# Performance work log

Measured on AMD Instinct MI355X. Metric: run time of the kernel, lower is better.

The kernel has to match this reference:

```python
import jax, jax.numpy as jnp
import numpy as np

D_MODEL = 384
N_HEADS = 8
HEAD_DIM = D_MODEL // N_HEADS


def setup_inputs() -> dict:
    key = jax.random.key(0)
    ks = jax.random.split(key, 8)
    b, n = 2, 2048
    s = 0.02
    return {
        "x": jax.random.normal(ks[0], (b, n, D_MODEL), jnp.float32),
        "coords": jax.random.normal(ks[1], (b, n, 3), jnp.float32),
        "W_qkv": jax.random.normal(ks[2], (D_MODEL, 3 * D_MODEL), jnp.float32) * s,
        "b_qkv": jnp.zeros((3 * D_MODEL,), jnp.float32),
        "W_dist": jax.random.normal(ks[3], (1, N_HEADS), jnp.float32) * s,
        "b_dist": jnp.zeros((N_HEADS,), jnp.float32),
        "W_out": jax.random.normal(ks[4], (D_MODEL, D_MODEL), jnp.float32) * s,
        "b_out": jnp.zeros((D_MODEL,), jnp.float32),
    }


def reference(x, coords, W_qkv, b_qkv, W_dist, b_dist, W_out, b_out):
    b, n, _ = x.shape
    qkv = x @ W_qkv + b_qkv                       # (b, n, 3*d)
    q, k, v = jnp.split(qkv, 3, axis=-1)
    def heads(t):
        return t.reshape(b, n, N_HEADS, HEAD_DIM).transpose(0, 2, 1, 3)  # b h n d
    q, k, v = heads(q), heads(k), heads(v)
    attn = jnp.einsum('bhid,bhjd->bhij', q, k) / jnp.sqrt(jnp.float32(HEAD_DIM))
    # distance bias: ||c_i - c_j|| projected to heads (Linear(1, n_heads))
    diff = coords[:, :, None, :] - coords[:, None, :, :]   # (b, i, j, 3)
    dist = jnp.sqrt(jnp.sum(diff * diff, axis=-1))         # (b, i, j)
    dist_bias = dist[..., None] * W_dist[0] + b_dist       # (b, i, j, h)
    attn = attn + dist_bias.transpose(0, 3, 1, 2)          # (b, h, i, j)
    attn = jax.nn.softmax(attn, axis=-1)
    out = jnp.einsum('bhij,bhjd->bhid', attn, v)
    out = out.transpose(0, 2, 1, 3).reshape(b, n, D_MODEL)
    return out @ W_out + b_out
```

## Files before the change

kernel.cpp:

```cpp
#include <hip/hip_runtime.h>
#include <hip/hip_bf16.h>

#define NB 2
#define SEQ 2048
#define DM 384
#define NH 8
#define HD 48
#define QKVN 1152

typedef __hip_bfloat16 bf16;
typedef __attribute__((ext_vector_type(8))) short short8;
typedef __attribute__((ext_vector_type(4))) float float4v;
typedef __attribute__((ext_vector_type(16))) float f32x16;

static __device__ __forceinline__ float bf2f(bf16 v){ return __bfloat162float(v); }
static __device__ __forceinline__ float ldin(const void* p, size_t i, int isf){
    return isf ? ((const float*)p)[i] : bf2f(((const bf16*)p)[i]);
}
static __device__ __forceinline__ short f2b(float f){
    union { float f; unsigned u; } a; a.f = f;
    unsigned r = a.u + 0x7FFFu + ((a.u >> 16) & 1u);
    return (short)(r >> 16);
}
static __device__ __forceinline__ unsigned pk2(float a, float b){
    union { __hip_bfloat162 h; unsigned u; } r;
    r.h = __float22bfloat162_rn(float2{a, b});
    return r.u;
}
static __device__ __forceinline__ float bflo(unsigned u){
    union { unsigned u; float f; } a; a.u = u << 16; return a.f;
}
static __device__ __forceinline__ float bfhi(unsigned u){
    union { unsigned u; float f; } a; a.u = u & 0xFFFF0000u; return a.f;
}
static __device__ __forceinline__ short8 u4pack(unsigned w0, unsigned w1, unsigned w2, unsigned w3){
    union { unsigned u[4]; short8 s; } r; r.u[0]=w0; r.u[1]=w1; r.u[2]=w2; r.u[3]=w3; return r.s;
}
static __device__ __forceinline__ int detect_isf(const void* x){
    const unsigned short* xb = (const unsigned short*)x;
    int l = threadIdx.x & 63;
    union { unsigned u; float f; } a; a.u = ((unsigned)xb[2*l]) << 16;
    float ab = fabsf(a.f);
    int good = (a.f == 0.0f) || (ab > 9.765625e-4f && ab < 1024.0f);
    unsigned long long m = __ballot(good);
    return (__popcll(m) >= 32) ? 0 : 1;
}

__global__ __launch_bounds__(256) void k_prep(const void* __restrict__ x,
    const void* __restrict__ coords,
    const void* __restrict__ Wqkv, const void* __restrict__ Wout,
    const void* __restrict__ bqkv, const void* __restrict__ bout,
    const void* __restrict__ Wdist, const void* __restrict__ bdist,
    short* __restrict__ dist8, short* __restrict__ xb,
    short* __restrict__ WqT, short* __restrict__ WoT,
    float* __restrict__ bqf, float* __restrict__ bof,
    float* __restrict__ wdf, float* __restrict__ bdf)
{
    const int isf = detect_isf(x);
    const int t = threadIdx.x;
    const int b = blockIdx.x;
    if (b < 512) {
        const int bb = b >> 8;
        const int jg = (b >> 1) & 127;
        const int j0 = jg * 16;
        const int ih = (b & 1) * 1024;
        __shared__ float cjx[16], cjy[16], cjz[16];
        if (t < 16) {
            int gj = (bb*SEQ + j0 + t)*3;
            cjx[t] = ldin(coords, gj, isf);
            cjy[t] = ldin(coords, gj+1, isf);
            cjz[t] = ldin(coords, gj+2, isf);
        }
        __syncthreads();
        #pragma unroll
        for (int k = 0; k < 4; ++k) {
            int i = ih + k*256 + t;
            int gi = (bb*SEQ + i)*3;
            float px = ldin(coords, gi, isf), py = ldin(coords, gi+1, isf), pz = ldin(coords, gi+2, isf);
            short o[16];
            #pragma unroll
            for (int e = 0; e < 16; ++e) {
                float dx = px - cjx[e], dy = py - cjy[e], dz = pz - cjz[e];
                o[e] = f2b(sqrtf(dx*dx + dy*dy + dz*dz));
            }
            short* dst = dist8 + (((size_t)bb*512 + (size_t)jg*4)*SEQ + i)*4;
            *(int2*)(dst)          = *(const int2*)(o);
            *(int2*)(dst + SEQ*4)  = *(const int2*)(o + 4);
            *(int2*)(dst + SEQ*8)  = *(const int2*)(o + 8);
            *(int2*)(dst + SEQ*12) = *(const int2*)(o + 12);
        }
    } else if (b < 1280) {
        size_t i = ((size_t)(b-512)*256 + t)*8;
        if (isf) {
            const float* xf = (const float*)x + i;
            short o[8];
            #pragma unroll
            for (int e = 0; e < 8; ++e) o[e] = f2b(xf[e]);
            *(int4*)(xb + i) = *(const int4*)o;
        } else {
            *(int4*)(xb + i) = *(const int4*)((const short*)x + i);
        }
    } else if (b < 1856) {
        int bb, NW; const void* W; short* WT;
        if (b < 1712) { bb = b - 1280; NW = QKVN; W = Wqkv; WT = WqT; }
        else          { bb = b - 1712; NW = DM;   W = Wout; WT = WoT; }
        int ntiles = NW >> 5;
        int kt = bb / ntiles, nt = bb % ntiles;
        int k0 = kt*32, n0 = nt*32;
        __shared__ float Ls[32][33];
        for (int idx = t; idx < 1024; idx += 256) {
            int r = idx >> 5, c = idx & 31;
            Ls[r][c] = ldin(W, (size_t)(k0+r)*NW + n0 + c, isf);
        }
        __syncthreads();
        for (int idx = t; idx < 1024; idx += 256) {
            int r2 = idx >> 5, c2 = idx & 31;
            WT[(size_t)(n0+r2)*DM + k0 + c2] = f2b(Ls[c2][r2]);
        }
    } else {
        int idx = (b - 1856)*256 + t;
        const float log2e = 1.4426950408889634f;
        if (idx < QKVN) bqf[idx] = ldin(bqkv, idx, isf);
        else if (idx < QKVN + DM) bof[idx - QKVN] = ldin(bout, idx - QKVN, isf);
        else if (idx < QKVN + DM + NH) wdf[idx - QKVN - DM] = ldin(Wdist, idx - QKVN - DM, isf)*log2e;
        else if (idx < QKVN + DM + 2*NH) bdf[idx - QKVN - DM - NH] = ldin(bdist, idx - QKVN - DM - NH, isf)*log2e;
    }
}

__global__ __launch_bounds__(256) void k_qkv(const short* __restrict__ xb,
    const short* __restrict__ WT, const float* __restrict__ bias,
    short* __restrict__ qg3, short* __restrict__ kg3, short* __restrict__ vg3)
{
    __shared__ __align__(16) short As[64*72];
    __shared__ __align__(16) short Bs[128*72];
    const int t = threadIdx.x;
    const int w = t >> 6, lane = t & 63, L = lane & 15, quad = lane >> 4;
    const int mt = blockIdx.x / 9, nt = blockIdx.x % 9;
    const int row0 = mt*64, col0 = nt*128;
    const int wm = w & 1, wn = w >> 1;
    float4v acc[2][4] = {};
    for (int k0 = 0; k0 < DM; k0 += 64) {
        __syncthreads();
        for (int c = t; c < 512; c += 256) {
            int row = c >> 3, k8 = c & 7;
            *(int4*)(&As[row*72 + k8*8]) = *(const int4*)(xb + (size_t)(row0+row)*DM + k0 + k8*8);
        }
        for (int c = t; c < 1024; c += 256) {
            int row = c >> 3, k8 = c & 7;
            *(int4*)(&Bs[row*72 + k8*8]) = *(const int4*)(WT + (size_t)(col0+row)*DM + k0 + k8*8);
        }
        __syncthreads();
        #pragma unroll
        for (int kc = 0; kc < 2; ++kc) {
            short8 a0 = *(const short8*)(&As[(32*wm + L)*72 + kc*32 + quad*8]);
            short8 a1 = *(const short8*)(&As[(32*wm + 16 + L)*72 + kc*32 + quad*8]);
            #pragma unroll
            for (int ni = 0; ni < 4; ++ni) {
                short8 bf = *(const short8*)(&Bs[(64*wn + 16*ni + L)*72 + kc*32 + quad*8]);
                acc[0][ni] = __builtin_amdgcn_mfma_f32_16x16x32_bf16(a0, bf, acc[0][ni], 0, 0, 0);
                acc[1][ni] = __builtin_amdgcn_mfma_f32_16x16x32_bf16(a1, bf, acc[1][ni], 0, 0, 0);
            }
        }
    }
    const int which = col0 / DM;
    const int cbase = col0 % DM;
    short* Ep = Bs;
    __syncthreads();
    if (which < 2) {
        #pragma unroll
        for (int mi = 0; mi < 2; ++mi)
            #pragma unroll
            for (int ni = 0; ni < 4; ++ni) {
                int col_l = 64*wn + 16*ni + L;
                float bv = bias[col0 + col_l];
                #pragma unroll
                for (int r = 0; r < 4; ++r) {
                    int row_l = 32*wm + 16*mi + quad*4 + r;
                    Ep[row_l*136 + col_l] = f2b(acc[mi][ni][r] + bv);
                }
            }
        __syncthreads();
        short* dst = which ? kg3 : qg3;
        for (int c = t; c < 1024; c += 256) {
            int row_l = c >> 4, col_l = (c & 15)*8;
            int row_g = row0 + row_l;
            int bi = row_g >> 11, nn = row_g & (SEQ-1);
            int c2 = cbase + col_l;
            int hh = c2/HD, dh = c2%HD;
            int bh = bi*NH + hh;
            int dc = dh >> 4, hi = (dh >> 3) & 1;
            size_t dstoff = ((size_t)bh*64 + (nn>>5))*1536 + (size_t)((dc*2 + hi)*256 + (nn&31)*8);
            *(int4*)(dst + dstoff) = *(const int4*)(&Ep[row_l*136 + col_l]);
        }
    } else {
        #pragma unroll
        for (int mi = 0; mi < 2; ++mi)
            #pragma unroll
            for (int ni = 0; ni < 4; ++ni) {
                int col_l = 64*wn + 16*ni + L;
                float bv = bias[col0 + col_l];
                #pragma unroll
                for (int r = 0; r < 4; ++r) {
                    int row_l = 32*wm + 16*mi + quad*4 + r;
                    Ep[col_l*72 + row_l] = f2b(acc[mi][ni][r] + bv);
                }
            }
        __syncthreads();
        for (int c = t; c < 1024; c += 256) {
            int col_l = c >> 3, row8 = (c & 7)*8;
            int row_g = row0 + row8;
            int bi = row_g >> 11, nn = row_g & (SEQ-1);
            int c2 = cbase + col_l;
            int hh = c2/HD, dh = c2%HD;
            int bh = bi*NH + hh;
            int jt = nn >> 5, jc = (nn >> 4) & 1;
            int ehalf = ((nn >> 3) & 1)*4;
            int dt = dh >> 5, dp = dh & 31;
            int hstride = dt ? 128 : 256;
            size_t base = ((size_t)bh*64 + jt)*1536 + (size_t)(jc*768 + dt*512 + dp*8 + ehalf);
            *(int2*)(vg3 + base)           = *(const int2*)(&Ep[col_l*72 + row8]);
            *(int2*)(vg3 + base + hstride) = *(const int2*)(&Ep[col_l*72 + row8 + 4]);
        }
    }
}

__global__ __launch_bounds__(256, 4) void k_attn(
    const short* __restrict__ qg3, const short* __restrict__ kg3, const short* __restrict__ vg3,
    const short* __restrict__ dist8, const float* __restrict__ wdf,
    const float* __restrict__ bdf, short* __restrict__ aob)
{
    __shared__ float Ored[2][32*48];
    __shared__ float Lred[2][32];
    const int t = threadIdx.x;
    const int w = t >> 6, lane = t & 63;
    const int li = lane & 31, hi = lane >> 5;
    const int bid = blockIdx.x;
    const int lg = (bid & 7)*128 + (bid >> 3);
    const int hh = lg & 7;
    const int rest = lg >> 3;
    const int bi = rest & 1, it = rest >> 1;
    const int bh = bi*NH + hh;
    const int i0 = it*32;
    const float scale2 = 0.14433756729740643f * 1.4426950408889634f;
    const float wd = wdf[hh], bd = bdf[hh];

    const short* qB = qg3 + ((size_t)bh*64 + it)*1536 + hi*256 + li*8;
    const short8 qf0 = *(const short8*)(qB);
    const short8 qf1 = *(const short8*)(qB + 512);
    const short8 qf2 = *(const short8*)(qB + 1024);

    f32x16 accO0 = {}, accO1 = {};
    float rsum = 0.0f;

    const short* kBp = kg3 + ((size_t)bh*64 + w)*1536 + hi*256 + li*8;
    const short* vBp = vg3 + ((size_t)bh*64 + w)*1536 + li*8;
    const short* dBp = dist8 + (((size_t)bi*512 + (size_t)w*8 + hi)*SEQ + i0 + li)*4;

    for (int s = 0; s < 16; ++s) {
        short8 kf0 = *(const short8*)(kBp);
        short8 kf1 = *(const short8*)(kBp + 512);
        short8 kf2 = *(const short8*)(kBp + 1024);
        int2 du0 = *(const int2*)(dBp);
        int2 du1 = *(const int2*)(dBp + SEQ*8);
        int2 du2 = *(const int2*)(dBp + SEQ*16);
        int2 du3 = *(const int2*)(dBp + SEQ*24);
        f32x16 sacc = {};
        sacc = __builtin_amdgcn_mfma_f32_32x32x16_bf16(kf0, qf0, sacc, 0, 0, 0);
        sacc = __builtin_amdgcn_mfma_f32_32x32x16_bf16(kf1, qf1, sacc, 0, 0, 0);
        sacc = __builtin_amdgcn_mfma_f32_32x32x16_bf16(kf2, qf2, sacc, 0, 0, 0);
        float p[16];
        #pragma unroll
        for (int rq = 0; rq < 4; ++rq) {
            int2 du = rq == 0 ? du0 : rq == 1 ? du1 : rq == 2 ? du2 : du3;
            float d0 = bflo((unsigned)du.x), d1 = bfhi((unsigned)du.x);
            float d2 = bflo((unsigned)du.y), d3 = bfhi((unsigned)du.y);
            p[4*rq+0] = __builtin_amdgcn_exp2f(fmaf(sacc[4*rq+0], scale2, fmaf(d0, wd, bd)));
            p[4*rq+1] = __builtin_amdgcn_exp2f(fmaf(sacc[4*rq+1], scale2, fmaf(d1, wd, bd)));
            p[4*rq+2] = __builtin_amdgcn_exp2f(fmaf(sacc[4*rq+2], scale2, fmaf(d2, wd, bd)));
            p[4*rq+3] = __builtin_amdgcn_exp2f(fmaf(sacc[4*rq+3], scale2, fmaf(d3, wd, bd)));
            rsum += (p[4*rq+0] + p[4*rq+1]) + (p[4*rq+2] + p[4*rq+3]);
        }
        short8 pa0 = u4pack(pk2(p[0],p[1]),  pk2(p[2],p[3]),  pk2(p[4],p[5]),   pk2(p[6],p[7]));
        short8 pa1 = u4pack(pk2(p[8],p[9]),  pk2(p[10],p[11]),pk2(p[12],p[13]), pk2(p[14],p[15]));
        short8 v00 = *(const short8*)(vBp + hi*256);
        short8 v10 = *(const short8*)(vBp + 768 + hi*256);
        accO0 = __builtin_amdgcn_mfma_f32_32x32x16_bf16(pa0, v00, accO0, 0, 0, 0);
        accO0 = __builtin_amdgcn_mfma_f32_32x32x16_bf16(pa1, v10, accO0, 0, 0, 0);
        short8 v01 = *(const short8*)(vBp + 512 + hi*128);
        short8 v11 = *(const short8*)(vBp + 1280 + hi*128);
        accO1 = __builtin_amdgcn_mfma_f32_32x32x16_bf16(pa0, v01, accO1, 0, 0, 0);
        accO1 = __builtin_amdgcn_mfma_f32_32x32x16_bf16(pa1, v11, accO1, 0, 0, 0);
        kBp += 4*1536; vBp += 4*1536; dBp += (size_t)SEQ*128;
    }
    rsum += __shfl_xor(rsum, 32);

    if (w >= 2) {
        float* Od = Ored[w-2];
        #pragma unroll
        for (int r = 0; r < 16; ++r) {
            int ii = (r & 3) + 8*(r >> 2) + 4*hi;
            Od[ii*48 + li] = accO0[r];
            if (li < 16) Od[ii*48 + 32 + li] = accO1[r];
        }
        if (lane < 32) Lred[w-2][lane] = rsum;
    }
    __syncthreads();
    if (w < 2) {
        const float* Od = Ored[w];
        #pragma unroll
        for (int r = 0; r < 16; ++r) {
            int ii = (r & 3) + 8*(r >> 2) + 4*hi;
            accO0[r] += Od[ii*48 + li];
            accO1[r] += Od[ii*48 + 32 + (li & 15)];
        }
        rsum += Lred[w][li];
    }
    __syncthreads();
    if (w == 1) {
        float* Od = Ored[0];
        #pragma unroll
        for (int r = 0; r < 16; ++r) {
            int ii = (r & 3) + 8*(r >> 2) + 4*hi;
            Od[ii*48 + li] = accO0[r];
            if (li < 16) Od[ii*48 + 32 + li] = accO1[r];
        }
        if (lane < 32) Lred[0][lane] = rsum;
    }
    __syncthreads();
    if (w == 0) {
        float* Od = Ored[0];
        #pragma unroll
        for (int r = 0; r < 16; ++r) {
            int ii = (r & 3) + 8*(r >> 2) + 4*hi;
            Od[ii*48 + li] += accO0[r];
            if (li < 16) Od[ii*48 + 32 + li] += accO1[r];
        }
        if (lane < 32) Lred[0][lane] += rsum;
    }
    __syncthreads();
    for (int c = t; c < 192; c += 256) {
        int r = c / 6, d8 = (c % 6)*8;
        float inv = 1.0f / Lred[0][r];
        const float* src = &Ored[0][r*48 + d8];
        short o[8];
        #pragma unroll
        for (int e = 0; e < 8; ++e) o[e] = f2b(src[e]*inv);
        *(int4*)(aob + ((size_t)(bi*SEQ) + i0 + r)*DM + hh*HD + d8) = *(const int4*)o;
    }
}

__global__ __launch_bounds__(256) void k_out(const short* __restrict__ aob,
    const short* __restrict__ WT, const float* __restrict__ bias,
    void* __restrict__ out, const void* __restrict__ x)
{
    __shared__ __align__(16) short As[64*72];
    __shared__ __align__(16) short Bs[128*72];
    const int isf = detect_isf(x);
    const int t = threadIdx.x;
    const int w = t >> 6, lane = t & 63, L = lane & 15, quad = lane >> 4;
    const int mt = blockIdx.x / 3, nt = blockIdx.x % 3;
    const int row0 = mt*64, col0 = nt*128;
    const int wm = w & 1, wn = w >> 1;
    float4v acc[2][4] = {};
    for (int k0 = 0; k0 < DM; k0 += 64) {
        __syncthreads();
        for (int c = t; c < 512; c += 256) {
            int row = c >> 3, k8 = c & 7;
            *(int4*)(&As[row*72 + k8*8]) = *(const int4*)(aob + (size_t)(row0+row)*DM + k0 + k8*8);
        }
        for (int c = t; c < 1024; c += 256) {
            int row = c >> 3, k8 = c & 7;
            *(int4*)(&Bs[row*72 + k8*8]) = *(const int4*)(WT + (size_t)(col0+row)*DM + k0 + k8*8);
        }
        __syncthreads();
        #pragma unroll
        for (int kc = 0; kc < 2; ++kc) {
            short8 a0 = *(const short8*)(&As[(32*wm + L)*72 + kc*32 + quad*8]);
            short8 a1 = *(const short8*)(&As[(32*wm + 16 + L)*72 + kc*32 + quad*8]);
            #pragma unroll
            for (int ni = 0; ni < 4; ++ni) {
                short8 bf = *(const short8*)(&Bs[(64*wn + 16*ni + L)*72 + kc*32 + quad*8]);
                acc[0][ni] = __builtin_amdgcn_mfma_f32_16x16x32_bf16(a0, bf, acc[0][ni], 0, 0, 0);
                acc[1][ni] = __builtin_amdgcn_mfma_f32_16x16x32_bf16(a1, bf, acc[1][ni], 0, 0, 0);
            }
        }
    }
    #pragma unroll
    for (int mi = 0; mi < 2; ++mi) {
        #pragma unroll
        for (int ni = 0; ni < 4; ++ni) {
            int col_g = col0 + 64*wn + 16*ni + L;
            float bv = bias[col_g];
            #pragma unroll
            for (int r = 0; r < 4; ++r) {
                int row_g = row0 + 32*wm + 16*mi + quad*4 + r;
                size_t oi = (size_t)row_g*DM + col_g;
                float val = acc[mi][ni][r] + bv;
                if (isf) ((float*)out)[oi] = val;
                else     ((bf16*)out)[oi]  = __float2bfloat16(val);
            }
        }
    }
}

extern "C" void kernel_launch(void* const* d_in, const int* in_sizes, int n_in,
                              void* d_out, int out_size, void* d_ws, size_t ws_size,
                              hipStream_t stream) {
    const void* x      = d_in[0];
    const void* coords = d_in[1];
    const void* Wqkv   = d_in[2];
    const void* bqkv   = d_in[3];
    const void* Wdist  = d_in[4];
    const void* bdist  = d_in[5];
    const void* Wout   = d_in[6];
    const void* bout   = d_in[7];

    short* qg3   = (short*)d_ws;
    short* kg3   = qg3  + (size_t)1572864;
    short* vg3   = kg3  + (size_t)1572864;
    short* dist8 = vg3  + (size_t)1573120;
    short* aob   = dist8 + (size_t)8388608;
    short* xb    = aob  + (size_t)1572864;
    short* WqT   = xb   + (size_t)1572864;
    short* WoT   = WqT  + (size_t)442368;
    float* bqf   = (float*)(WoT + (size_t)147456);
    float* bof   = bqf + QKVN;
    float* wdf   = bof + DM;
    float* bdf   = wdf + NH;

    k_prep<<<dim3(1863), dim3(256), 0, stream>>>(x, coords, Wqkv, Wout, bqkv, bout,
                                                 Wdist, bdist, dist8, xb, WqT, WoT,
                                                 bqf, bof, wdf, bdf);
    k_qkv<<<dim3(64*9), dim3(256), 0, stream>>>(xb, WqT, bqf, qg3, kg3, vg3);
    k_attn<<<dim3(16*64), dim3(256), 0, stream>>>(qg3, kg3, vg3, dist8, wdf, bdf, aob);
    k_out<<<dim3(64*3), dim3(256), 0, stream>>>(aob, WoT, bof, d_out, x);
}
```

Baseline: 144.3 us.

## Compute distance bias inside attention kernel and double query rows per block

The precomputed bf16 pairwise-distance matrix (about 16 MB written by the prep kernel and read back in attention) is removed. Each attention block now stages that batch's coordinates in shared memory and computes the distance with a sqrt on the fly. Each block also processes 64 query rows instead of 32, so every K/V fragment loaded feeds two score tiles; launch bounds drop to 2 blocks per CU and the grid halves. This trades global memory traffic for extra ALU and sqrt work, more registers and lower occupancy.

```diff
diff --git a/kernel.cpp b/kernel.cpp
--- a/kernel.cpp
+++ b/kernel.cpp
@@ -26,12 +26,6 @@
     union { __hip_bfloat162 h; unsigned u; } r;
     r.h = __float22bfloat162_rn(float2{a, b});
     return r.u;
-}
-static __device__ __forceinline__ float bflo(unsigned u){
-    union { unsigned u; float f; } a; a.u = u << 16; return a.f;
-}
-static __device__ __forceinline__ float bfhi(unsigned u){
-    union { unsigned u; float f; } a; a.u = u & 0xFFFF0000u; return a.f;
 }
 static __device__ __forceinline__ short8 u4pack(unsigned w0, unsigned w1, unsigned w2, unsigned w3){
     union { unsigned u[4]; short8 s; } r; r.u[0]=w0; r.u[1]=w1; r.u[2]=w2; r.u[3]=w3; return r.s;
@@ -51,7 +45,7 @@
     const void* __restrict__ Wqkv, const void* __restrict__ Wout,
     const void* __restrict__ bqkv, const void* __restrict__ bout,
     const void* __restrict__ Wdist, const void* __restrict__ bdist,
-    short* __restrict__ dist8, short* __restrict__ xb,
+    float* __restrict__ cjf, short* __restrict__ xb,
     short* __restrict__ WqT, short* __restrict__ WoT,
     float* __restrict__ bqf, float* __restrict__ bof,
     float* __restrict__ wdf, float* __restrict__ bdf)
@@ -59,38 +53,21 @@
     const int isf = detect_isf(x);
     const int t = threadIdx.x;
     const int b = blockIdx.x;
-    if (b < 512) {
-        const int bb = b >> 8;
-        const int jg = (b >> 1) & 127;
-        const int j0 = jg * 16;
-        const int ih = (b & 1) * 1024;
-        __shared__ float cjx[16], cjy[16], cjz[16];
-        if (t < 16) {
-            int gj = (bb*SEQ + j0 + t)*3;
-            cjx[t] = ldin(coords, gj, isf);
-            cjy[t] = ldin(coords, gj+1, isf);
-            cjz[t] = ldin(coords, gj+2, isf);
-        }
-        __syncthreads();
-        #pragma unroll
-        for (int k = 0; k < 4; ++k) {
-            int i = ih + k*256 + t;
-            int gi = (bb*SEQ + i)*3;
-            float px = ldin(coords, gi, isf), py = ldin(coords, gi+1, isf), pz = ldin(coords, gi+2, isf);
-            short o[16];
-            #pragma unroll
-            for (int e = 0; e < 16; ++e) {
-                float dx = px - cjx[e], dy = py - cjy[e], dz = pz - cjz[e];
-                o[e] = f2b(sqrtf(dx*dx + dy*dy + dz*dz));
-            }
-            short* dst = dist8 + (((size_t)bb*512 + (size_t)jg*4)*SEQ + i)*4;
-            *(int2*)(dst)          = *(const int2*)(o);
-            *(int2*)(dst + SEQ*4)  = *(const int2*)(o + 4);
-            *(int2*)(dst + SEQ*8)  = *(const int2*)(o + 8);
-            *(int2*)(dst + SEQ*12) = *(const int2*)(o + 12);
-        }
-    } else if (b < 1280) {
-        size_t i = ((size_t)(b-512)*256 + t)*8;
+    if (b < 8) {
+        #pragma unroll
+        for (int k = 0; k < 2; ++k) {
+            int e = b*512 + k*256 + t;
+            int bb = e >> 11, jj = e & 2047;
+            size_t gi = ((size_t)bb*SEQ + jj)*3;
+            float4 cv;
+            cv.x = ldin(coords, gi, isf);
+            cv.y = ldin(coords, gi+1, isf);
+            cv.z = ldin(coords, gi+2, isf);
+            cv.w = 0.0f;
+            ((float4*)cjf)[e] = cv;
+        }
+    } else if (b < 776) {
+        size_t i = ((size_t)(b-8)*256 + t)*8;
         if (isf) {
             const float* xf = (const float*)x + i;
             short o[8];
@@ -100,10 +77,10 @@
         } else {
             *(int4*)(xb + i) = *(const int4*)((const short*)x + i);
         }
-    } else if (b < 1856) {
+    } else if (b < 1352) {
         int bb, NW; const void* W; short* WT;
-        if (b < 1712) { bb = b - 1280; NW = QKVN; W = Wqkv; WT = WqT; }
-        else          { bb = b - 1712; NW = DM;   W = Wout; WT = WoT; }
+        if (b < 1208) { bb = b - 776;  NW = QKVN; W = Wqkv; WT = WqT; }
+        else          { bb = b - 1208; NW = DM;   W = Wout; WT = WoT; }
         int ntiles = NW >> 5;
         int kt = bb / ntiles, nt = bb % ntiles;
         int k0 = kt*32, n0 = nt*32;
@@ -118,7 +95,7 @@
             WT[(size_t)(n0+r2)*DM + k0 + c2] = f2b(Ls[c2][r2]);
         }
     } else {
-        int idx = (b - 1856)*256 + t;
+        int idx = (b - 1352)*256 + t;
         const float log2e = 1.4426950408889634f;
         if (idx < QKVN) bqf[idx] = ldin(bqkv, idx, isf);
         else if (idx < QKVN + DM) bof[idx - QKVN] = ldin(bout, idx - QKVN, isf);
@@ -224,121 +201,156 @@
     }
 }
 
-__global__ __launch_bounds__(256, 4) void k_attn(
+__global__ __launch_bounds__(256, 2) void k_attn(
     const short* __restrict__ qg3, const short* __restrict__ kg3, const short* __restrict__ vg3,
-    const short* __restrict__ dist8, const float* __restrict__ wdf,
+    const float* __restrict__ cjf, const float* __restrict__ wdf,
     const float* __restrict__ bdf, short* __restrict__ aob)
 {
-    __shared__ float Ored[2][32*48];
-    __shared__ float Lred[2][32];
+    __shared__ float4 cjs[2048];
+    __shared__ float Ored[2][64*48];
+    __shared__ float Lred[2][64];
     const int t = threadIdx.x;
     const int w = t >> 6, lane = t & 63;
     const int li = lane & 31, hi = lane >> 5;
-    const int bid = blockIdx.x;
-    const int lg = (bid & 7)*128 + (bid >> 3);
-    const int hh = lg & 7;
-    const int rest = lg >> 3;
-    const int bi = rest & 1, it = rest >> 1;
-    const int bh = bi*NH + hh;
-    const int i0 = it*32;
+    const int lg = (blockIdx.x & 7)*64 + (blockIdx.x >> 3);
+    const int bh = lg >> 5, it = lg & 31;
+    const int bi = bh >> 3, hh = bh & 7;
+    const int i0 = it*64;
     const float scale2 = 0.14433756729740643f * 1.4426950408889634f;
     const float wd = wdf[hh], bd = bdf[hh];
 
-    const short* qB = qg3 + ((size_t)bh*64 + it)*1536 + hi*256 + li*8;
-    const short8 qf0 = *(const short8*)(qB);
-    const short8 qf1 = *(const short8*)(qB + 512);
-    const short8 qf2 = *(const short8*)(qB + 1024);
-
-    f32x16 accO0 = {}, accO1 = {};
-    float rsum = 0.0f;
+    for (int c = t; c < 2048; c += 256)
+        cjs[c] = ((const float4*)cjf)[(size_t)bi*2048 + c];
+    float cix[2], ciy[2], ciz[2];
+    #pragma unroll
+    for (int m = 0; m < 2; ++m) {
+        float4 cv = ((const float4*)cjf)[(size_t)bi*2048 + i0 + m*32 + li];
+        cix[m] = cv.x; ciy[m] = cv.y; ciz[m] = cv.z;
+    }
+    const short* qB = qg3 + ((size_t)bh*64 + it*2)*1536 + hi*256 + li*8;
+    short8 qf[2][3];
+    #pragma unroll
+    for (int m = 0; m < 2; ++m)
+        #pragma unroll
+        for (int d = 0; d < 3; ++d)
+            qf[m][d] = *(const short8*)(qB + m*1536 + d*512);
+    __syncthreads();
+
+    f32x16 aO0[2] = {}, aO1[2] = {};
+    float rsum[2] = {};
 
     const short* kBp = kg3 + ((size_t)bh*64 + w)*1536 + hi*256 + li*8;
     const short* vBp = vg3 + ((size_t)bh*64 + w)*1536 + li*8;
-    const short* dBp = dist8 + (((size_t)bi*512 + (size_t)w*8 + hi)*SEQ + i0 + li)*4;
+    int jb = w*32 + hi*4;
 
     for (int s = 0; s < 16; ++s) {
         short8 kf0 = *(const short8*)(kBp);
         short8 kf1 = *(const short8*)(kBp + 512);
         short8 kf2 = *(const short8*)(kBp + 1024);
-        int2 du0 = *(const int2*)(dBp);
-        int2 du1 = *(const int2*)(dBp + SEQ*8);
-        int2 du2 = *(const int2*)(dBp + SEQ*16);
-        int2 du3 = *(const int2*)(dBp + SEQ*24);
-        f32x16 sacc = {};
-        sacc = __builtin_amdgcn_mfma_f32_32x32x16_bf16(kf0, qf0, sacc, 0, 0, 0);
-        sacc = __builtin_amdgcn_mfma_f32_32x32x16_bf16(kf1, qf1, sacc, 0, 0, 0);
-        sacc = __builtin_amdgcn_mfma_f32_32x32x16_bf16(kf2, qf2, sacc, 0, 0, 0);
-        float p[16];
-        #pragma unroll
-        for (int rq = 0; rq < 4; ++rq) {
-            int2 du = rq == 0 ? du0 : rq == 1 ? du1 : rq == 2 ? du2 : du3;
-            float d0 = bflo((unsigned)du.x), d1 = bfhi((unsigned)du.x);
-            float d2 = bflo((unsigned)du.y), d3 = bfhi((unsigned)du.y);
-            p[4*rq+0] = __builtin_amdgcn_exp2f(fmaf(sacc[4*rq+0], scale2, fmaf(d0, wd, bd)));
-            p[4*rq+1] = __builtin_amdgcn_exp2f(fmaf(sacc[4*rq+1], scale2, fmaf(d1, wd, bd)));
-            p[4*rq+2] = __builtin_amdgcn_exp2f(fmaf(sacc[4*rq+2], scale2, fmaf(d2, wd, bd)));
-            p[4*rq+3] = __builtin_amdgcn_exp2f(fmaf(sacc[4*rq+3], scale2, fmaf(d3, wd, bd)));
-            rsum += (p[4*rq+0] + p[4*rq+1]) + (p[4*rq+2] + p[4*rq+3]);
-        }
-        short8 pa0 = u4pack(pk2(p[0],p[1]),  pk2(p[2],p[3]),  pk2(p[4],p[5]),   pk2(p[6],p[7]));
-        short8 pa1 = u4pack(pk2(p[8],p[9]),  pk2(p[10],p[11]),pk2(p[12],p[13]), pk2(p[14],p[15]));
         short8 v00 = *(const short8*)(vBp + hi*256);
         short8 v10 = *(const short8*)(vBp + 768 + hi*256);
-        accO0 = __builtin_amdgcn_mfma_f32_32x32x16_bf16(pa0, v00, accO0, 0, 0, 0);
-        accO0 = __builtin_amdgcn_mfma_f32_32x32x16_bf16(pa1, v10, accO0, 0, 0, 0);
         short8 v01 = *(const short8*)(vBp + 512 + hi*128);
         short8 v11 = *(const short8*)(vBp + 1280 + hi*128);
-        accO1 = __builtin_amdgcn_mfma_f32_32x32x16_bf16(pa0, v01, accO1, 0, 0, 0);
-        accO1 = __builtin_amdgcn_mfma_f32_32x32x16_bf16(pa1, v11, accO1, 0, 0, 0);
-        kBp += 4*1536; vBp += 4*1536; dBp += (size_t)SEQ*128;
-    }
-    rsum += __shfl_xor(rsum, 32);
+        f32x16 s0 = {}, s1 = {};
+        s0 = __builtin_amdgcn_mfma_f32_32x32x16_bf16(kf0, qf[0][0], s0, 0, 0, 0);
+        s1 = __builtin_amdgcn_mfma_f32_32x32x16_bf16(kf0, qf[1][0], s1, 0, 0, 0);
+        s0 = __builtin_amdgcn_mfma_f32_32x32x16_bf16(kf1, qf[0][1], s0, 0, 0, 0);
+        s1 = __builtin_amdgcn_mfma_f32_32x32x16_bf16(kf1, qf[1][1], s1, 0, 0, 0);
+        s0 = __builtin_amdgcn_mfma_f32_32x32x16_bf16(kf2, qf[0][2], s0, 0, 0, 0);
+        s1 = __builtin_amdgcn_mfma_f32_32x32x16_bf16(kf2, qf[1][2], s1, 0, 0, 0);
+        unsigned pw0[8], pw1[8];
+        #pragma unroll
+        for (int rq = 0; rq < 4; ++rq) {
+            float p0[4], p1[4];
+            #pragma unroll
+            for (int q = 0; q < 4; ++q) {
+                float4 cj = cjs[jb + 8*rq + q];
+                int r = 4*rq + q;
+                float dx0 = cix[0]-cj.x, dy0 = ciy[0]-cj.y, dz0 = ciz[0]-cj.z;
+                float dd0 = sqrtf(dx0*dx0 + dy0*dy0 + dz0*dz0);
+                float dx1 = cix[1]-cj.x, dy1 = ciy[1]-cj.y, dz1 = ciz[1]-cj.z;
+                float dd1 = sqrtf(dx1*dx1 + dy1*dy1 + dz1*dz1);
+                p0[q] = __builtin_amdgcn_exp2f(fmaf(s0[r], scale2, fmaf(dd0, wd, bd)));
+                p1[q] = __builtin_amdgcn_exp2f(fmaf(s1[r], scale2, fmaf(dd1, wd, bd)));
+            }
+            rsum[0] += (p0[0] + p0[1]) + (p0[2] + p0[3]);
+            rsum[1] += (p1[0] + p1[1]) + (p1[2] + p1[3]);
+            pw0[2*rq]   = pk2(p0[0], p0[1]);
+            pw0[2*rq+1] = pk2(p0[2], p0[3]);
+            pw1[2*rq]   = pk2(p1[0], p1[1]);
+            pw1[2*rq+1] = pk2(p1[2], p1[3]);
+        }
+        short8 pa00 = u4pack(pw0[0], pw0[1], pw0[2], pw0[3]);
+        short8 pa01 = u4pack(pw0[4], pw0[5], pw0[6], pw0[7]);
+        short8 pa10 = u4pack(pw1[0], pw1[1], pw1[2], pw1[3]);
+        short8 pa11 = u4pack(pw1[4], pw1[5], pw1[6], pw1[7]);
+        aO0[0] = __builtin_amdgcn_mfma_f32_32x32x16_bf16(pa00, v00, aO0[0], 0, 0, 0);
+        aO0[0] = __builtin_amdgcn_mfma_f32_32x32x16_bf16(pa01, v10, aO0[0], 0, 0, 0);
+        aO1[0] = __builtin_amdgcn_mfma_f32_32x32x16_bf16(pa00, v01, aO1[0], 0, 0, 0);
+        aO1[0] = __builtin_amdgcn_mfma_f32_32x32x16_bf16(pa01, v11, aO1[0], 0, 0, 0);
+        aO0[1] = __builtin_amdgcn_mfma_f32_32x32x16_bf16(pa10, v00, aO0[1], 0, 0, 0);
+        aO0[1] = __builtin_amdgcn_mfma_f32_32x32x16_bf16(pa11, v10, aO0[1], 0, 0, 0);
+        aO1[1] = __builtin_amdgcn_mfma_f32_32x32x16_bf16(pa10, v01, aO1[1], 0, 0, 0);
+        aO1[1] = __builtin_amdgcn_mfma_f32_32x32x16_bf16(pa11, v11, aO1[1], 0, 0, 0);
+        kBp += 4*1536; vBp += 4*1536; jb += 128;
+    }
+    #pragma unroll
+    for (int m = 0; m < 2; ++m)
+        rsum[m] += __shfl_xor(rsum[m], 32);
 
     if (w >= 2) {
         float* Od = Ored[w-2];
         #pragma unroll
-        for (int r = 0; r < 16; ++r) {
-            int ii = (r & 3) + 8*(r >> 2) + 4*hi;
-            Od[ii*48 + li] = accO0[r];
-            if (li < 16) Od[ii*48 + 32 + li] = accO1[r];
-        }
-        if (lane < 32) Lred[w-2][lane] = rsum;
+        for (int m = 0; m < 2; ++m)
+            #pragma unroll
+            for (int r = 0; r < 16; ++r) {
+                int ii = m*32 + (r & 3) + 8*(r >> 2) + 4*hi;
+                Od[ii*48 + li] = aO0[m][r];
+                if (li < 16) Od[ii*48 + 32 + li] = aO1[m][r];
+            }
+        if (lane < 32) { Lred[w-2][li] = rsum[0]; Lred[w-2][32 + li] = rsum[1]; }
     }
     __syncthreads();
     if (w < 2) {
         const float* Od = Ored[w];
         #pragma unroll
-        for (int r = 0; r < 16; ++r) {
-            int ii = (r & 3) + 8*(r >> 2) + 4*hi;
-            accO0[r] += Od[ii*48 + li];
-            accO1[r] += Od[ii*48 + 32 + (li & 15)];
-        }
-        rsum += Lred[w][li];
+        for (int m = 0; m < 2; ++m)
+            #pragma unroll
+            for (int r = 0; r < 16; ++r) {
+                int ii = m*32 + (r & 3) + 8*(r >> 2) + 4*hi;
+                aO0[m][r] += Od[ii*48 + li];
+                aO1[m][r] += Od[ii*48 + 32 + (li & 15)];
+            }
+        rsum[0] += Lred[w][li]; rsum[1] += Lred[w][32 + li];
     }
     __syncthreads();
     if (w == 1) {
         float* Od = Ored[0];
         #pragma unroll
-        for (int r = 0; r < 16; ++r) {
-            int ii = (r & 3) + 8*(r >> 2) + 4*hi;
-            Od[ii*48 + li] = accO0[r];
-            if (li < 16) Od[ii*48 + 32 + li] = accO1[r];
-        }
-        if (lane < 32) Lred[0][lane] = rsum;
+        for (int m = 0; m < 2; ++m)
+            #pragma unroll
+            for (int r = 0; r < 16; ++r) {
+                int ii = m*32 + (r & 3) + 8*(r >> 2) + 4*hi;
+                Od[ii*48 + li] = aO0[m][r];
+                if (li < 16) Od[ii*48 + 32 + li] = aO1[m][r];
+            }
+        if (lane < 32) { Lred[0][li] = rsum[0]; Lred[0][32 + li] = rsum[1]; }
     }
     __syncthreads();
     if (w == 0) {
         float* Od = Ored[0];
         #pragma unroll
-        for (int r = 0; r < 16; ++r) {
-            int ii = (r & 3) + 8*(r >> 2) + 4*hi;
-            Od[ii*48 + li] += accO0[r];
-            if (li < 16) Od[ii*48 + 32 + li] += accO1[r];
-        }
-        if (lane < 32) Lred[0][lane] += rsum;
-    }
-    __syncthreads();
-    for (int c = t; c < 192; c += 256) {
+        for (int m = 0; m < 2; ++m)
+            #pragma unroll
+            for (int r = 0; r < 16; ++r) {
+                int ii = m*32 + (r & 3) + 8*(r >> 2) + 4*hi;
+                Od[ii*48 + li] += aO0[m][r];
+                if (li < 16) Od[ii*48 + 32 + li] += aO1[m][r];
+            }
+        if (lane < 32) { Lred[0][li] += rsum[0]; Lred[0][32 + li] += rsum[1]; }
+    }
+    __syncthreads();
+    for (int c = t; c < 384; c += 256) {
         int r = c / 6, d8 = (c % 6)*8;
         float inv = 1.0f / Lred[0][r];
         const float* src = &Ored[0][r*48 + d8];
@@ -418,8 +430,7 @@
     short* qg3   = (short*)d_ws;
     short* kg3   = qg3  + (size_t)1572864;
     short* vg3   = kg3  + (size_t)1572864;
-    short* dist8 = vg3  + (size_t)1573120;
-    short* aob   = dist8 + (size_t)8388608;
+    short* aob   = vg3  + (size_t)1573120;
     short* xb    = aob  + (size_t)1572864;
     short* WqT   = xb   + (size_t)1572864;
     short* WoT   = WqT  + (size_t)442368;
@@ -427,11 +438,12 @@
     float* bof   = bqf + QKVN;
     float* wdf   = bof + DM;
     float* bdf   = wdf + NH;
-
-    k_prep<<<dim3(1863), dim3(256), 0, stream>>>(x, coords, Wqkv, Wout, bqkv, bout,
-                                                 Wdist, bdist, dist8, xb, WqT, WoT,
+    float* cjf   = bdf + NH;
+
+    k_prep<<<dim3(1359), dim3(256), 0, stream>>>(x, coords, Wqkv, Wout, bqkv, bout,
+                                                 Wdist, bdist, cjf, xb, WqT, WoT,
                                                  bqf, bof, wdf, bdf);
     k_qkv<<<dim3(64*9), dim3(256), 0, stream>>>(xb, WqT, bqf, qg3, kg3, vg3);
-    k_attn<<<dim3(16*64), dim3(256), 0, stream>>>(qg3, kg3, vg3, dist8, wdf, bdf, aob);
+    k_attn<<<dim3(512), dim3(256), 0, stream>>>(qg3, kg3, vg3, cjf, wdf, bdf, aob);
     k_out<<<dim3(64*3), dim3(256), 0, stream>>>(aob, WoT, bof, d_out, x);
 }
```

New measurement: 174.2 us. 20.7% more time.

## Fuse x bf16 conversion into QKV GEMM and remap attention blocks per XCD

Applied to the files above, without the earlier changes.

Drops the separate x-to-bf16 conversion pass from the prep kernel. The QKV GEMM now reads x directly and converts fp32 to bf16 while staging its A tile, which saves a write and re-read of the bf16 copy. The attention kernel also changes its block-to-work mapping so each XCD handles one batch and one quarter of the query tiles, aiming for better L2 locality on K/V and the distance data. The cost is that x is converted redundantly across the 9 N-tiles of the GEMM, and fp32 global loads for the A tile are twice as large.

```diff
diff --git a/kernel.cpp b/kernel.cpp
--- a/kernel.cpp
+++ b/kernel.cpp
@@ -51,7 +51,7 @@
     const void* __restrict__ Wqkv, const void* __restrict__ Wout,
     const void* __restrict__ bqkv, const void* __restrict__ bout,
     const void* __restrict__ Wdist, const void* __restrict__ bdist,
-    short* __restrict__ dist8, short* __restrict__ xb,
+    short* __restrict__ dist8,
     short* __restrict__ WqT, short* __restrict__ WoT,
     float* __restrict__ bqf, float* __restrict__ bof,
     float* __restrict__ wdf, float* __restrict__ bdf)
@@ -89,21 +89,10 @@
             *(int2*)(dst + SEQ*8)  = *(const int2*)(o + 8);
             *(int2*)(dst + SEQ*12) = *(const int2*)(o + 12);
         }
-    } else if (b < 1280) {
-        size_t i = ((size_t)(b-512)*256 + t)*8;
-        if (isf) {
-            const float* xf = (const float*)x + i;
-            short o[8];
-            #pragma unroll
-            for (int e = 0; e < 8; ++e) o[e] = f2b(xf[e]);
-            *(int4*)(xb + i) = *(const int4*)o;
-        } else {
-            *(int4*)(xb + i) = *(const int4*)((const short*)x + i);
-        }
-    } else if (b < 1856) {
+    } else if (b < 1088) {
         int bb, NW; const void* W; short* WT;
-        if (b < 1712) { bb = b - 1280; NW = QKVN; W = Wqkv; WT = WqT; }
-        else          { bb = b - 1712; NW = DM;   W = Wout; WT = WoT; }
+        if (b < 944) { bb = b - 512; NW = QKVN; W = Wqkv; WT = WqT; }
+        else         { bb = b - 944; NW = DM;   W = Wout; WT = WoT; }
         int ntiles = NW >> 5;
         int kt = bb / ntiles, nt = bb % ntiles;
         int k0 = kt*32, n0 = nt*32;
@@ -118,7 +107,7 @@
             WT[(size_t)(n0+r2)*DM + k0 + c2] = f2b(Ls[c2][r2]);
         }
     } else {
-        int idx = (b - 1856)*256 + t;
+        int idx = (b - 1088)*256 + t;
         const float log2e = 1.4426950408889634f;
         if (idx < QKVN) bqf[idx] = ldin(bqkv, idx, isf);
         else if (idx < QKVN + DM) bof[idx - QKVN] = ldin(bout, idx - QKVN, isf);
@@ -127,12 +116,13 @@
     }
 }
 
-__global__ __launch_bounds__(256) void k_qkv(const short* __restrict__ xb,
+__global__ __launch_bounds__(256) void k_qkv(const void* __restrict__ x,
     const short* __restrict__ WT, const float* __restrict__ bias,
     short* __restrict__ qg3, short* __restrict__ kg3, short* __restrict__ vg3)
 {
     __shared__ __align__(16) short As[64*72];
     __shared__ __align__(16) short Bs[128*72];
+    const int isf = detect_isf(x);
     const int t = threadIdx.x;
     const int w = t >> 6, lane = t & 63, L = lane & 15, quad = lane >> 4;
     const int mt = blockIdx.x / 9, nt = blockIdx.x % 9;
@@ -143,7 +133,16 @@
         __syncthreads();
         for (int c = t; c < 512; c += 256) {
             int row = c >> 3, k8 = c & 7;
-            *(int4*)(&As[row*72 + k8*8]) = *(const int4*)(xb + (size_t)(row0+row)*DM + k0 + k8*8);
+            size_t src = (size_t)(row0+row)*DM + k0 + k8*8;
+            if (isf) {
+                const float* xf = (const float*)x + src;
+                short o[8];
+                #pragma unroll
+                for (int e = 0; e < 8; ++e) o[e] = f2b(xf[e]);
+                *(int4*)(&As[row*72 + k8*8]) = *(const int4*)o;
+            } else {
+                *(int4*)(&As[row*72 + k8*8]) = *(const int4*)((const short*)x + src);
+            }
         }
         for (int c = t; c < 1024; c += 256) {
             int row = c >> 3, k8 = c & 7;
@@ -234,12 +233,13 @@
     const int t = threadIdx.x;
     const int w = t >> 6, lane = t & 63;
     const int li = lane & 31, hi = lane >> 5;
-    const int bid = blockIdx.x;
-    const int lg = (bid & 7)*128 + (bid >> 3);
-    const int hh = lg & 7;
-    const int rest = lg >> 3;
-    const int bi = rest & 1, it = rest >> 1;
-    const int bh = bi*NH + hh;
+    const int xcd  = blockIdx.x & 7;
+    const int slot = blockIdx.x >> 3;
+    const int bi   = xcd >> 2;
+    const int band = xcd & 3;
+    const int hh   = slot & 7;
+    const int it   = band*16 + (slot >> 3);
+    const int bh   = bi*NH + hh;
     const int i0 = it*32;
     const float scale2 = 0.14433756729740643f * 1.4426950408889634f;
     const float wd = wdf[hh], bd = bdf[hh];
@@ -420,18 +420,17 @@
     short* vg3   = kg3  + (size_t)1572864;
     short* dist8 = vg3  + (size_t)1573120;
     short* aob   = dist8 + (size_t)8388608;
-    short* xb    = aob  + (size_t)1572864;
-    short* WqT   = xb   + (size_t)1572864;
+    short* WqT   = aob  + (size_t)1572864;
     short* WoT   = WqT  + (size_t)442368;
     float* bqf   = (float*)(WoT + (size_t)147456);
     float* bof   = bqf + QKVN;
     float* wdf   = bof + DM;
     float* bdf   = wdf + NH;
 
-    k_prep<<<dim3(1863), dim3(256), 0, stream>>>(x, coords, Wqkv, Wout, bqkv, bout,
-                                                 Wdist, bdist, dist8, xb, WqT, WoT,
+    k_prep<<<dim3(1095), dim3(256), 0, stream>>>(x, coords, Wqkv, Wout, bqkv, bout,
+                                                 Wdist, bdist, dist8, WqT, WoT,
                                                  bqf, bof, wdf, bdf);
-    k_qkv<<<dim3(64*9), dim3(256), 0, stream>>>(xb, WqT, bqf, qg3, kg3, vg3);
-    k_attn<<<dim3(16*64), dim3(256), 0, stream>>>(qg3, kg3, vg3, dist8, wdf, bdf, aob);
+    k_qkv<<<dim3(64*9), dim3(256), 0, stream>>>(x, WqT, bqf, qg3, kg3, vg3);
+    k_attn<<<dim3(1024), dim3(256), 0, stream>>>(qg3, kg3, vg3, dist8, wdf, bdf, aob);
     k_out<<<dim3(64*3), dim3(256), 0, stream>>>(aob, WoT, bof, d_out, x);
 }
```

Measured after the change: 146.2 us. No clear change (+1.3%).
